# Kernel tuning notes

Measured on AMD Instinct MI355X. Metric: run time of the kernel, lower is better.

## Reference

```python
import jax, jax.numpy as jnp
from jax import lax
import numpy as np

B, T, C = 4, 2048, 1024
H = 4                      # num_heads
D = C // H                 # head_dim
EPS_N = 1e-6               # normalizer eps in scan
EPS_GN = 1e-5              # GroupNorm eps (torch default)


def setup_inputs() -> dict:
    key = jax.random.key(0)
    ks = jax.random.split(key, 8)
    s = 0.02
    return {
        "x": jax.random.normal(ks[0], (B, T, C), jnp.float32),
        "conv_w": jax.random.normal(ks[1], (C, 1, 4), jnp.float32) * s,
        "conv_b": jax.random.normal(ks[2], (C,), jnp.float32) * s,
        "wx_w": jax.random.normal(ks[3], (4 * C, C), jnp.float32) * s,
        "wx_b": jax.random.normal(ks[4], (4 * C,), jnp.float32) * s,
        "gn_w": jnp.ones((C,), jnp.float32),
        "gn_b": jnp.zeros((C,), jnp.float32),
        "out_w": jax.random.normal(ks[5], (C, C), jnp.float32) * s,
        "out_b": jax.random.normal(ks[6], (C,), jnp.float32) * s,
    }


def _slstm_scan(i_g, f_g, z_g, o_g):
    # all inputs (B,T,H,D); scan over time
    def step(carry, g):
        c, n, m = carry
        i_t, f_t, z_t, o_t = g
        m_t = jnp.maximum(f_t + m, i_t)
        i_p = jnp.exp(i_t - m_t)
        f_p = jnp.exp(f_t + m - m_t)
        c_t = f_p * c + i_p * z_t
        n_t = f_p * n + i_p
        h_t = jax.nn.sigmoid(o_t) * (c_t / (n_t + EPS_N))
        return (c_t, n_t, m_t), h_t

    tfirst = lambda a: jnp.transpose(a, (1, 0, 2, 3))  # (T,B,H,D)
    init = (jnp.zeros((B, H, D), i_g.dtype),
            jnp.ones((B, H, D), i_g.dtype),
            jnp.zeros((B, H, D), i_g.dtype))
    _, h_seq = lax.scan(step, init, (tfirst(i_g), tfirst(f_g), tfirst(z_g), tfirst(o_g)))
    return jnp.transpose(h_seq, (1, 0, 2, 3))  # (B,T,H,D)


def reference(x, conv_w, conv_b, wx_w, wx_b, gn_w, gn_b, out_w, out_b):
    # causal depthwise conv (torch pad=3 both sides, sliced to first T == left pad 3)
    xc = jnp.transpose(x, (0, 2, 1))  # (B,C,T)
    xc = lax.conv_general_dilated(
        xc, conv_w, window_strides=(1,), padding=[(3, 0)],
        dimension_numbers=("NCH", "OIH", "NCH"), feature_group_count=C)
    xc = jax.nn.silu(xc + conv_b[None, :, None])
    xc = jnp.transpose(xc, (0, 2, 1))  # (B,T,C)

    gates = jnp.einsum("btc,gc->btg", xc, wx_w) + wx_b  # (B,T,4C)
    gates = gates.reshape(B, T, 4, H, D)
    i_g, f_g, z_g, o_g = (gates[:, :, k] for k in range(4))
    z_g = jnp.tanh(z_g)

    h = _slstm_scan(i_g, f_g, z_g, o_g).reshape(B, T, C)

    # GroupNorm(H groups) over (B,C,T): normalize per (batch, group) over (D, T)
    hg = h.reshape(B, T, H, D)
    mean = hg.mean(axis=(1, 3), keepdims=True)
    var = hg.var(axis=(1, 3), keepdims=True)
    hn = ((hg - mean) / jnp.sqrt(var + EPS_GN)).reshape(B, T, C)
    hn = hn * gn_w + gn_b

    out = jnp.einsum("btc,oc->bto", hn, out_w) + out_b
    return out + x  # dropout is identity at inference
```

## Files before the change

### kernel.cpp

```cpp
#include <hip/hip_runtime.h>

#define B_ 4
#define T_ 2048
#define C_ 1024
#define H_ 4
#define D_ 256
#define M_ (B_*T_)
#define N1_ (4*C_)
#define K_ C_
#define LANES_ (B_*C_)
#define CHUNK_ 32
#define NCHUNK_ (T_/CHUNK_)

typedef unsigned short u16;
typedef unsigned int u32;
typedef __bf16 bf16x8 __attribute__((ext_vector_type(8)));
typedef float f32x4 __attribute__((ext_vector_type(4)));
typedef float vf4 __attribute__((ext_vector_type(4)));
typedef unsigned short u16x4 __attribute__((ext_vector_type(4)));
typedef unsigned short u16x8 __attribute__((ext_vector_type(8)));

__device__ __forceinline__ u16 f2bf(float f) {
  union { float f; u32 u; } v; v.f = f;
  u32 u = v.u;
  u32 r = (u + 0x7FFFu + ((u >> 16) & 1u)) >> 16;
  return (u16)r;
}
__device__ __forceinline__ float b2f(u16 h) {
  union { u32 u; float f; } v; v.u = ((u32)h) << 16;
  return v.f;
}

#define NCAST_ ((N1_*K_ + C_*C_) / 2048)

__global__ void prep_kernel(const float* __restrict__ wx_w, const float* __restrict__ out_w,
                            u16* __restrict__ w1p, u16* __restrict__ w2,
                            const float* __restrict__ x, const float* __restrict__ cw,
                            const float* __restrict__ cb, u16* __restrict__ xc,
                            float* __restrict__ stats) {
  if (blockIdx.x < NCAST_) {
    int i8 = (blockIdx.x * 256 + threadIdx.x) * 8;
    u16x8 o;
    if (i8 < N1_ * K_) {
      int n = i8 >> 10, k8 = i8 & 1023;
      const float* src = wx_w + (size_t)(((n & 3) << 10) | (n >> 2)) * K_ + k8;
      vf4 a = *(const vf4*)src;
      vf4 b = *(const vf4*)(src + 4);
#pragma unroll
      for (int j = 0; j < 4; ++j) { o[j] = f2bf(a[j]); o[j + 4] = f2bf(b[j]); }
      *(u16x8*)(w1p + i8) = o;
    } else {
      int j8 = i8 - N1_ * K_;
      vf4 a = *(const vf4*)(out_w + j8);
      vf4 b = *(const vf4*)(out_w + j8 + 4);
#pragma unroll
      for (int j = 0; j < 4; ++j) { o[j] = f2bf(a[j]); o[j + 4] = f2bf(b[j]); }
      *(u16x8*)(w2 + j8) = o;
    }
    return;
  }
  if (blockIdx.x == NCAST_ && threadIdx.x < 32) stats[threadIdx.x] = 0.f;
  int i4 = ((blockIdx.x - NCAST_) * 256 + threadIdx.x) * 4;
  int c = i4 & (C_ - 1);
  int t = (i4 >> 10) & (T_ - 1);
  vf4 acc = *(const vf4*)(cb + c);
  vf4 w0 = *(const vf4*)(cw + (size_t)c * 4);
  vf4 w1 = *(const vf4*)(cw + (size_t)(c + 1) * 4);
  vf4 w2v = *(const vf4*)(cw + (size_t)(c + 2) * 4);
  vf4 w3 = *(const vf4*)(cw + (size_t)(c + 3) * 4);
#pragma unroll
  for (int k = 0; k < 4; ++k) {
    if (t - 3 + k >= 0) {
      vf4 xv = *(const vf4*)(x + (size_t)i4 + (size_t)(k - 3) * C_);
      acc[0] = fmaf(w0[k], xv[0], acc[0]);
      acc[1] = fmaf(w1[k], xv[1], acc[1]);
      acc[2] = fmaf(w2v[k], xv[2], acc[2]);
      acc[3] = fmaf(w3[k], xv[3], acc[3]);
    }
  }
  u16x4 o;
#pragma unroll
  for (int j = 0; j < 4; ++j) {
    float s = acc[j] / (1.f + __expf(-acc[j]));
    o[j] = f2bf(s);
  }
  *(u16x4*)(xc + i4) = o;
}

template <int EPI>
__global__ __launch_bounds__(256, 3)
void gemm_bt(const u16* __restrict__ A, const u16* __restrict__ Bw,
             const float* __restrict__ bias, const float* __restrict__ resid,
             u16* __restrict__ obf, float* __restrict__ of32,
             f32x4* __restrict__ sSum, int M, int N, int K)
{
  __shared__ __align__(16) u16 smem[128 * 136];
  u16* a_s = smem;
  u16* b_s = smem + 128 * 64;

  const int tid  = threadIdx.x;
  const int lane = tid & 63;
  const int l15  = lane & 15;
  const int q    = lane >> 4;
  const int wave = tid >> 6;
  const int wm   = (wave >> 1) * 64;
  const int wn   = (wave & 1) * 64;
  const int bm   = blockIdx.y * 128;
  const int bn   = blockIdx.x * 128;

  const int srow   = wave * 8 + (lane >> 3);
  const int schunk = lane & 7;

  float bias4[4];
#pragma unroll
  for (int sn = 0; sn < 4; ++sn) {
    int gcol = bn + wn + sn * 16 + l15;
    bias4[sn] = (EPI == 0) ? bias[((gcol & 3) << 10) | (gcol >> 2)] : bias[gcol];
  }
  const bool zlane = (EPI == 0) && ((l15 & 3) == 2);

  f32x4 acc[4][4];
#pragma unroll
  for (int i = 0; i < 4; ++i)
#pragma unroll
    for (int j = 0; j < 4; ++j) acc[i][j] = (f32x4){0.f, 0.f, 0.f, 0.f};

  for (int k0 = 0; k0 < K; k0 += 64) {
#pragma unroll
    for (int i = 0; i < 4; ++i) {
      int r = i * 32 + srow;
      int lc = schunk ^ (r & 7);
      const u16* ga = A  + (size_t)(bm + r) * K + k0 + lc * 8;
      const u16* gb = Bw + (size_t)(bn + r) * K + k0 + lc * 8;
      __builtin_amdgcn_global_load_lds(
          (const __attribute__((address_space(1))) u32*)ga,
          (__attribute__((address_space(3))) u32*)&a_s[(i * 32 + wave * 8) * 64],
          16, 0, 0);
      __builtin_amdgcn_global_load_lds(
          (const __attribute__((address_space(1))) u32*)gb,
          (__attribute__((address_space(3))) u32*)&b_s[(i * 32 + wave * 8) * 64],
          16, 0, 0);
    }
    __syncthreads();
#pragma unroll
    for (int kk = 0; kk < 64; kk += 32) {
      const int kc = kk >> 3;
      bf16x8 af[4], bfr[4];
#pragma unroll
      for (int s = 0; s < 4; ++s) {
        int ra = wm + s * 16 + l15;
        int ph = (kc + q) ^ (ra & 7);
        af[s] = *(const bf16x8*)&a_s[ra * 64 + ph * 8];
      }
#pragma unroll
      for (int s = 0; s < 4; ++s) {
        int rb = wn + s * 16 + l15;
        int ph = (kc + q) ^ (rb & 7);
        bfr[s] = *(const bf16x8*)&b_s[rb * 64 + ph * 8];
      }
#pragma unroll
      for (int sm = 0; sm < 4; ++sm)
#pragma unroll
        for (int sn = 0; sn < 4; ++sn)
          acc[sm][sn] = __builtin_amdgcn_mfma_f32_16x16x32_bf16(af[sm], bfr[sn], acc[sm][sn], 0, 0, 0);
    }
    __syncthreads();
  }

  if (EPI == 0) {
#pragma unroll
    for (int smi = 0; smi < 4; ++smi) {
#pragma unroll
      for (int r = 0; r < 4; ++r) {
        int lrow = wm + smi * 16 + q * 4 + r;
#pragma unroll
        for (int sni = 0; sni < 4; ++sni) {
          int lcol = wn + sni * 16 + l15;
          float v = acc[smi][sni][r] + bias4[sni];
          if (zlane) {
            float e = __expf(2.f * v);
            v = (e - 1.f) / (e + 1.f);
          }
          smem[lrow * 136 + lcol] = f2bf(v);
        }
      }
    }
    __syncthreads();
#pragma unroll
    for (int it = 0; it < 8; ++it) {
      int flat = it * 256 + tid;
      int row = flat >> 4;
      int ch  = flat & 15;
      u16x8 vv = *(const u16x8*)&smem[row * 136 + ch * 8];
      *(u16x8*)(obf + (size_t)(bm + row) * N + bn + ch * 8) = vv;
    }
    if (tid < 128) {
      int ch = tid & 31, ck = tid >> 5;
      const u16* sp = smem + (ck * 32) * 136 + ch * 4;
      float F = 0.f, Mx = -1e30f, aBc = 0.f, aBn = 0.f;
#pragma unroll 8
      for (int t = 0; t < CHUNK_; ++t) {
        u16x4 gv = *(const u16x4*)(sp + t * 136);
        float i_t = b2f(gv[0]), f_t = b2f(gv[1]), z_t = b2f(gv[2]);
        float Mf = Mx + f_t;
        float Mn = fmaxf(Mf, i_t);
        float ea = __expf(Mf - Mn), eb = __expf(i_t - Mn);
        aBc = ea * aBc + eb * z_t;
        aBn = ea * aBn + eb;
        F += f_t; Mx = Mn;
      }
      int b = bm >> 11;
      int s = ((bm & 2047) >> 5) + ck;
      int cg = (bn >> 2) + ch;
      sSum[(size_t)s * LANES_ + b * C_ + cg] = (f32x4){F, Mx, aBc, aBn};
    }
  } else {
    float* fs = (float*)smem;
#pragma unroll
    for (int h = 0; h < 2; ++h) {
      __syncthreads();
#pragma unroll
      for (int smi2 = 0; smi2 < 2; ++smi2) {
        int smi = 2 * h + smi2;
#pragma unroll
        for (int r = 0; r < 4; ++r) {
          int slot = (wm >> 1) + smi2 * 16 + q * 4 + r;
#pragma unroll
          for (int sni = 0; sni < 4; ++sni) {
            int lcol = wn + sni * 16 + l15;
            fs[slot * 132 + lcol] = acc[smi][sni][r] + bias4[sni];
          }
        }
      }
      __syncthreads();
#pragma unroll
      for (int it = 0; it < 8; ++it) {
        int flat = it * 256 + tid;
        int slot = flat >> 5;
        int c4 = (flat & 31) * 4;
        int absrow = bm + ((slot & 32) << 1) + (h << 5) + (slot & 31);
        vf4 v = *(const vf4*)&fs[slot * 132 + c4];
        vf4 rv = *(const vf4*)(resid + (size_t)absrow * N + bn + c4);
        v[0] += rv[0]; v[1] += rv[1]; v[2] += rv[2]; v[3] += rv[3];
        *(vf4*)(of32 + (size_t)absrow * N + bn + c4) = v;
      }
    }
  }
}

__global__ void scan_prefix(const f32x4* __restrict__ sSum, f32x4* __restrict__ iSt) {
  int l = blockIdx.x * 256 + threadIdx.x;
  float ct = 0.f, nt = 1.f, mt = 0.f;
#pragma unroll 8
  for (int s = 0; s < NCHUNK_; ++s) {
    int idx = s * LANES_ + l;
    f32x4 S = sSum[idx];
    iSt[idx] = (f32x4){ct, nt, mt, 0.f};
    float mf = mt + S[0];
    float mn = fmaxf(mf, S[1]);
    float a = __expf(mf - mn);
    float bcoef = __expf(S[1] - mn);
    ct = a * ct + bcoef * S[2];
    nt = a * nt + bcoef * S[3];
    mt = mn;
  }
}

__global__ void scan_passB(const u16* __restrict__ gates, const f32x4* __restrict__ iSt,
                           u16* __restrict__ h, float* __restrict__ stats) {
  int tid = blockIdx.x * 256 + threadIdx.x;
  int lp = tid & 2047;
  int s = tid >> 11;
  int b = lp >> 9;
  int c2 = (lp & 511) * 2;
  const u16* g = gates + ((size_t)(b * T_ + s * CHUNK_) * C_ + c2) * 4;
  u16* hp = h + (size_t)(b * T_ + s * CHUNK_) * C_ + c2;
  int idx = s * LANES_ + b * C_ + c2;
  f32x4 S0 = iSt[idx], S1 = iSt[idx + 1];
  float cc0 = S0[0], nn0 = S0[1], mm0 = S0[2];
  float cc1 = S1[0], nn1 = S1[1], mm1 = S1[2];
  float ls = 0.f, lq = 0.f;
#pragma unroll 4
  for (int t = 0; t < CHUNK_; ++t) {
    u16x8 gv = *(const u16x8*)(g + (size_t)t * C_ * 4);
    float h0, h1;
    {
      float i_t = b2f(gv[0]), f_t = b2f(gv[1]), z_t = b2f(gv[2]), o_t = b2f(gv[3]);
      float m_new = fmaxf(f_t + mm0, i_t);
      float i_p = __expf(i_t - m_new);
      float f_p = __expf(f_t + mm0 - m_new);
      cc0 = f_p * cc0 + i_p * z_t;
      nn0 = f_p * nn0 + i_p;
      mm0 = m_new;
      float sig_o = 1.f / (1.f + __expf(-o_t));
      h0 = sig_o * (cc0 / (nn0 + 1e-6f));
    }
    {
      float i_t = b2f(gv[4]), f_t = b2f(gv[5]), z_t = b2f(gv[6]), o_t = b2f(gv[7]);
      float m_new = fmaxf(f_t + mm1, i_t);
      float i_p = __expf(i_t - m_new);
      float f_p = __expf(f_t + mm1 - m_new);
      cc1 = f_p * cc1 + i_p * z_t;
      nn1 = f_p * nn1 + i_p;
      mm1 = m_new;
      float sig_o = 1.f / (1.f + __expf(-o_t));
      h1 = sig_o * (cc1 / (nn1 + 1e-6f));
    }
    u16 hb0 = f2bf(h0), hb1 = f2bf(h1);
    float v0 = b2f(hb0), v1 = b2f(hb1);
    ls += v0 + v1; lq += v0 * v0 + v1 * v1;
    *(u32*)(hp + (size_t)t * C_) = (u32)hb0 | ((u32)hb1 << 16);
  }
  __shared__ float rs[256], rq[256];
  int thr = threadIdx.x;
  rs[thr] = ls; rq[thr] = lq;
  __syncthreads();
  for (int off = 64; off > 0; off >>= 1) {
    if ((thr & 127) < off) { rs[thr] += rs[thr + off]; rq[thr] += rq[thr + off]; }
    __syncthreads();
  }
  if ((thr & 127) == 0) {
    int grp = b * 4 + (c2 >> 8);
    atomicAdd(&stats[grp * 2 + 0], rs[thr]);
    atomicAdd(&stats[grp * 2 + 1], rq[thr]);
  }
}

__global__ void norm_kernel(const u16* __restrict__ h, const float* __restrict__ stats,
                            const float* __restrict__ gn_w, const float* __restrict__ gn_b,
                            u16* __restrict__ hn) {
  int i8 = (blockIdx.x * 256 + threadIdx.x) * 8;
  int c = i8 & (C_ - 1);
  int b = i8 >> 21;
  int grp = b * 4 + (c >> 8);
  const float inv_n = 1.f / (float)(T_ * D_);
  float mean = stats[grp * 2 + 0] * inv_n;
  float var  = stats[grp * 2 + 1] * inv_n - mean * mean;
  float rstd = rsqrtf(var + 1e-5f);
  u16x8 hv = *(const u16x8*)(h + i8);
  vf4 w0 = *(const vf4*)(gn_w + c), w1 = *(const vf4*)(gn_w + c + 4);
  vf4 b0 = *(const vf4*)(gn_b + c), b1 = *(const vf4*)(gn_b + c + 4);
  u16x8 o;
#pragma unroll
  for (int j = 0; j < 4; ++j) {
    o[j]     = f2bf((b2f(hv[j])     - mean) * rstd * w0[j] + b0[j]);
    o[j + 4] = f2bf((b2f(hv[j + 4]) - mean) * rstd * w1[j] + b1[j]);
  }
  *(u16x8*)(hn + i8) = o;
}

extern "C" void kernel_launch(void* const* d_in, const int* in_sizes, int n_in,
                              void* d_out, int out_size, void* d_ws, size_t ws_size,
                              hipStream_t stream) {
  const float* x      = (const float*)d_in[0];
  const float* conv_w = (const float*)d_in[1];
  const float* conv_b = (const float*)d_in[2];
  const float* wx_w   = (const float*)d_in[3];
  const float* wx_b   = (const float*)d_in[4];
  const float* gn_w   = (const float*)d_in[5];
  const float* gn_b   = (const float*)d_in[6];
  const float* out_w  = (const float*)d_in[7];
  const float* out_b  = (const float*)d_in[8];
  float* out = (float*)d_out;

  char* p = (char*)d_ws;
  u16* xc    = (u16*)p; p += (size_t)M_ * K_ * 2;
  u16* w1    = (u16*)p; p += (size_t)N1_ * K_ * 2;
  u16* w2    = (u16*)p; p += (size_t)C_ * C_ * 2;
  u16* gts   = (u16*)p; p += (size_t)M_ * N1_ * 2;
  u16* hb    = (u16*)p; p += (size_t)M_ * C_ * 2;
  u16* hn    = (u16*)p; p += (size_t)M_ * C_ * 2;
  float* stats = (float*)p; p += 256;
  const int nsum = LANES_ * NCHUNK_;
  f32x4* sSum = (f32x4*)p; p += (size_t)nsum * 16;
  f32x4* iSt  = (f32x4*)p; p += (size_t)nsum * 16;

  prep_kernel<<<NCAST_ + (M_ * C_) / 1024, 256, 0, stream>>>(
      wx_w, out_w, w1, w2, x, conv_w, conv_b, xc, stats);

  gemm_bt<0><<<dim3(N1_ / 128, M_ / 128), 256, 0, stream>>>(
      xc, w1, wx_b, nullptr, gts, nullptr, sSum, M_, N1_, K_);

  scan_prefix<<<LANES_ / 256, 256, 0, stream>>>(sSum, iSt);
  scan_passB<<<(2048 * NCHUNK_) / 256, 256, 0, stream>>>(gts, iSt, hb, stats);

  norm_kernel<<<(M_ * C_) / 2048, 256, 0, stream>>>(hb, stats, gn_w, gn_b, hn);

  gemm_bt<1><<<dim3(C_ / 128, M_ / 128), 256, 0, stream>>>(
      hn, w2, out_b, x, nullptr, out, nullptr, M_, C_, K_);
}
```

Before: 268.2 us.

## Replace gates GEMM with 256x256-tile, 512-thread, 4-stage LDS-pipelined kernel

Adds a dedicated gates GEMM that uses 256x256 output tiles with 8 waves and a 4-buffer ring of direct global-to-LDS loads, staged three slices ahead. Counted vmcnt waits, barrier sandwiches and setprio around the MFMA bursts are meant to overlap loads with compute. The bias, tanh and chunk-summary epilogue is kept. Larger tiles increase data reuse and cut global traffic per FLOP. This uses about 132KB of LDS and many accumulator registers, which limits occupancy, and it hardcodes shapes and a block-swizzle mapping.

After: 281.6 us. 5.0% more time.

```diff
diff --git a/kernel.cpp b/kernel.cpp
--- a/kernel.cpp
+++ b/kernel.cpp
@@ -85,6 +85,182 @@
     o[j] = f2bf(s);
   }
   *(u16x4*)(xc + i4) = o;
+}
+
+
+__device__ __forceinline__ void stage32(const u16* __restrict__ G, int rowBase, int ks,
+                                        u16* dstPart, int wave, int lane) {
+#pragma unroll
+  for (int r = 0; r < 2; ++r) {
+    int R = r * 64 + wave * 8 + (lane >> 3);
+    int c = (lane & 7) ^ (R & 7);
+    int grow = 2 * R + (c >> 2);
+    int koff = ks * 32 + (c & 3) * 8;
+    const u16* src = G + (size_t)(rowBase + grow) * K_ + koff;
+    __builtin_amdgcn_global_load_lds(
+        (const __attribute__((address_space(1))) u32*)src,
+        (__attribute__((address_space(3))) u32*)&dstPart[(r * 64 + wave * 8) * 64],
+        16, 0, 0);
+  }
+}
+
+#define BARRIER_SANDWICH() do {                   \
+    __builtin_amdgcn_sched_barrier(0);            \
+    __builtin_amdgcn_s_barrier();                 \
+    __builtin_amdgcn_sched_barrier(0);            \
+  } while (0)
+
+#define VM8 asm volatile("s_waitcnt vmcnt(8)" ::: "memory")
+#define VM4 asm volatile("s_waitcnt vmcnt(4)" ::: "memory")
+#define VM0 asm volatile("s_waitcnt vmcnt(0)" ::: "memory")
+#define VMNONE ((void)0)
+
+#define GEMM_SLICE(sIdx, DO_STAGE, VMW) do {                                     \
+    u16* base_ = smem + ((sIdx) & 3) * 16384;                                    \
+    const u16* aP_ = base_;                                                      \
+    const u16* bP_ = base_ + 8192;                                               \
+    bf16x8 af_[4], bf_[4];                                                       \
+    _Pragma("unroll")                                                            \
+    for (int sub = 0; sub < 4; ++sub) {                                          \
+      int ra = wr * 128 + sub * 16 + l15;                                        \
+      int Ra = ra >> 1;                                                          \
+      int ca = (((ra & 1) << 2) | q) ^ (Ra & 7);                                 \
+      af_[sub] = *(const bf16x8*)&aP_[Ra * 64 + ca * 8];                         \
+      int rb = wc * 64 + sub * 16 + l15;                                         \
+      int Rb = rb >> 1;                                                          \
+      int cb = (((rb & 1) << 2) | q) ^ (Rb & 7);                                 \
+      bf_[sub] = *(const bf16x8*)&bP_[Rb * 64 + cb * 8];                         \
+    }                                                                            \
+    if (DO_STAGE) stage32(A, bm, (sIdx) + 3,                                     \
+        smem + (((sIdx) + 3) & 3) * 16384, wave, lane);                          \
+    BARRIER_SANDWICH();                                                          \
+    __builtin_amdgcn_s_setprio(1);                                               \
+    _Pragma("unroll")                                                            \
+    for (int sm = 0; sm < 4; ++sm)                                               \
+      _Pragma("unroll")                                                          \
+      for (int sn = 0; sn < 4; ++sn)                                             \
+        acc[sm][sn] = __builtin_amdgcn_mfma_f32_16x16x32_bf16(af_[sm], bf_[sn],  \
+                                                              acc[sm][sn], 0, 0, 0); \
+    __builtin_amdgcn_s_setprio(0);                                               \
+    BARRIER_SANDWICH();                                                          \
+    _Pragma("unroll")                                                            \
+    for (int sub = 0; sub < 4; ++sub) {                                          \
+      int ra = wr * 128 + 64 + sub * 16 + l15;                                   \
+      int Ra = ra >> 1;                                                          \
+      int ca = (((ra & 1) << 2) | q) ^ (Ra & 7);                                 \
+      af_[sub] = *(const bf16x8*)&aP_[Ra * 64 + ca * 8];                         \
+    }                                                                            \
+    if (DO_STAGE) stage32(Bw, bn, (sIdx) + 3,                                    \
+        smem + (((sIdx) + 3) & 3) * 16384 + 8192, wave, lane);                   \
+    BARRIER_SANDWICH();                                                          \
+    __builtin_amdgcn_s_setprio(1);                                               \
+    _Pragma("unroll")                                                            \
+    for (int sm = 0; sm < 4; ++sm)                                               \
+      _Pragma("unroll")                                                          \
+      for (int sn = 0; sn < 4; ++sn)                                             \
+        acc[4 + sm][sn] = __builtin_amdgcn_mfma_f32_16x16x32_bf16(af_[sm], bf_[sn], \
+                                                          acc[4 + sm][sn], 0, 0, 0); \
+    __builtin_amdgcn_s_setprio(0);                                               \
+    VMW;                                                                         \
+    BARRIER_SANDWICH();                                                          \
+  } while (0)
+
+__global__ __launch_bounds__(512, 2)
+void gemm256_gates(const u16* __restrict__ A, const u16* __restrict__ Bw,
+                   const float* __restrict__ bias,
+                   u16* __restrict__ obf, f32x4* __restrict__ sSum)
+{
+  __shared__ __align__(16) u16 smem[67584];
+
+  const int tid  = threadIdx.x;
+  const int lane = tid & 63;
+  const int l15  = lane & 15;
+  const int q    = lane >> 4;
+  const int wave = tid >> 6;
+  const int wr   = wave >> 2;
+  const int wc   = wave & 3;
+
+  const int bid = blockIdx.y * 16 + blockIdx.x;
+  const int swz = (bid & 7) * 64 + (bid >> 3);
+  const int bm = (swz >> 4) * 256;
+  const int bn = (swz & 15) * 256;
+
+  float bias4[4];
+#pragma unroll
+  for (int sn = 0; sn < 4; ++sn) {
+    int gcol = bn + wc * 64 + sn * 16 + l15;
+    bias4[sn] = bias[((gcol & 3) << 10) | (gcol >> 2)];
+  }
+  const bool zlane = ((l15 & 3) == 2);
+
+  f32x4 acc[8][4];
+#pragma unroll
+  for (int i = 0; i < 8; ++i)
+#pragma unroll
+    for (int j = 0; j < 4; ++j) acc[i][j] = (f32x4){0.f, 0.f, 0.f, 0.f};
+
+#pragma unroll
+  for (int s3 = 0; s3 < 3; ++s3) {
+    stage32(A,  bm, s3, smem + s3 * 16384,        wave, lane);
+    stage32(Bw, bn, s3, smem + s3 * 16384 + 8192, wave, lane);
+  }
+  asm volatile("s_waitcnt vmcnt(8)" ::: "memory");
+  BARRIER_SANDWICH();
+
+#pragma unroll 1
+  for (int s = 0; s < 29; ++s) GEMM_SLICE(s, true, VM8);
+  GEMM_SLICE(29, false, VM4);
+  GEMM_SLICE(30, false, VM0);
+  GEMM_SLICE(31, false, VMNONE);
+
+#pragma unroll
+  for (int sm = 0; sm < 8; ++sm) {
+#pragma unroll
+    for (int r = 0; r < 4; ++r) {
+      int lrow = wr * 128 + sm * 16 + q * 4 + r;
+#pragma unroll
+      for (int sn = 0; sn < 4; ++sn) {
+        int lcol = wc * 64 + sn * 16 + l15;
+        float v = acc[sm][sn][r] + bias4[sn];
+        if (zlane) {
+          float e = __expf(2.f * v);
+          v = (e - 1.f) / (e + 1.f);
+        }
+        smem[lrow * 264 + lcol] = f2bf(v);
+      }
+    }
+  }
+  __syncthreads();
+
+#pragma unroll
+  for (int it = 0; it < 16; ++it) {
+    int flat = it * 512 + tid;
+    int row = flat >> 5;
+    int ch8 = flat & 31;
+    u16x8 vv = *(const u16x8*)&smem[row * 264 + ch8 * 8];
+    *(u16x8*)(obf + (size_t)(bm + row) * N1_ + bn + ch8 * 8) = vv;
+  }
+
+  {
+    int ch = tid & 63, ck = tid >> 6;
+    const u16* sp = smem + (ck * 32) * 264 + ch * 4;
+    float F = 0.f, Mx = -1e30f, aBc = 0.f, aBn = 0.f;
+#pragma unroll 8
+    for (int t = 0; t < CHUNK_; ++t) {
+      u16x4 gv = *(const u16x4*)(sp + t * 264);
+      float i_t = b2f(gv[0]), f_t = b2f(gv[1]), z_t = b2f(gv[2]);
+      float Mf = Mx + f_t;
+      float Mn = fmaxf(Mf, i_t);
+      float ea = __expf(Mf - Mn), eb = __expf(i_t - Mn);
+      aBc = ea * aBc + eb * z_t;
+      aBn = ea * aBn + eb;
+      F += f_t; Mx = Mn;
+    }
+    int b = bm >> 11;
+    int s_ = ((bm & 2047) >> 5) + ck;
+    int cg = (bn >> 2) + ch;
+    sSum[(size_t)s_ * LANES_ + b * C_ + cg] = (f32x4){F, Mx, aBc, aBn};
+  }
 }
 
 template <int EPI>
@@ -378,8 +554,8 @@
   prep_kernel<<<NCAST_ + (M_ * C_) / 1024, 256, 0, stream>>>(
       wx_w, out_w, w1, w2, x, conv_w, conv_b, xc, stats);
 
-  gemm_bt<0><<<dim3(N1_ / 128, M_ / 128), 256, 0, stream>>>(
-      xc, w1, wx_b, nullptr, gts, nullptr, sSum, M_, N1_, K_);
+  gemm256_gates<<<dim3(N1_ / 256, M_ / 256), 512, 0, stream>>>(
+      xc, w1, wx_b, gts, sSum);
 
   scan_prefix<<<LANES_ / 256, 256, 0, stream>>>(sSum, iSt);
   scan_passB<<<(2048 * NCHUNK_) / 256, 256, 0, stream>>>(gts, iSt, hb, stats);
```

## Fold GroupNorm affine into per-batch output projection weights and bias

Applied to the files above, without the earlier changes.

Replaces the elementwise GroupNorm kernel, which read h and wrote a normalized copy, with a small kernel that folds mean, rstd, gamma and beta into per-batch scaled bf16 copies of out_w plus an adjusted bias. The output GEMM then reads the raw h buffer directly and selects the batch's weights and bias by row block. This removes a full read/write pass over the activation, and the out_w bf16 cast moves out of prep. In exchange it writes and reads four weight copies (8 MB) and applies the scale in bf16 weights rather than activations, which slightly changes rounding.

New measurement: 279.0 us (median of 2 runs). 1.04x slower.

```diff
diff --git a/kernel.cpp b/kernel.cpp
--- a/kernel.cpp
+++ b/kernel.cpp
@@ -31,32 +31,23 @@
   return v.f;
 }
 
-#define NCAST_ ((N1_*K_ + C_*C_) / 2048)
-
-__global__ void prep_kernel(const float* __restrict__ wx_w, const float* __restrict__ out_w,
-                            u16* __restrict__ w1p, u16* __restrict__ w2,
+#define NCAST_ ((N1_*K_) / 2048)
+
+__global__ void prep_kernel(const float* __restrict__ wx_w,
+                            u16* __restrict__ w1p,
                             const float* __restrict__ x, const float* __restrict__ cw,
                             const float* __restrict__ cb, u16* __restrict__ xc,
                             float* __restrict__ stats) {
   if (blockIdx.x < NCAST_) {
     int i8 = (blockIdx.x * 256 + threadIdx.x) * 8;
+    int n = i8 >> 10, k8 = i8 & 1023;
+    const float* src = wx_w + (size_t)(((n & 3) << 10) | (n >> 2)) * K_ + k8;
+    vf4 a = *(const vf4*)src;
+    vf4 b = *(const vf4*)(src + 4);
     u16x8 o;
-    if (i8 < N1_ * K_) {
-      int n = i8 >> 10, k8 = i8 & 1023;
-      const float* src = wx_w + (size_t)(((n & 3) << 10) | (n >> 2)) * K_ + k8;
-      vf4 a = *(const vf4*)src;
-      vf4 b = *(const vf4*)(src + 4);
-#pragma unroll
-      for (int j = 0; j < 4; ++j) { o[j] = f2bf(a[j]); o[j + 4] = f2bf(b[j]); }
-      *(u16x8*)(w1p + i8) = o;
-    } else {
-      int j8 = i8 - N1_ * K_;
-      vf4 a = *(const vf4*)(out_w + j8);
-      vf4 b = *(const vf4*)(out_w + j8 + 4);
-#pragma unroll
-      for (int j = 0; j < 4; ++j) { o[j] = f2bf(a[j]); o[j + 4] = f2bf(b[j]); }
-      *(u16x8*)(w2 + j8) = o;
-    }
+#pragma unroll
+    for (int j = 0; j < 4; ++j) { o[j] = f2bf(a[j]); o[j + 4] = f2bf(b[j]); }
+    *(u16x8*)(w1p + i8) = o;
     return;
   }
   if (blockIdx.x == NCAST_ && threadIdx.x < 32) stats[threadIdx.x] = 0.f;
@@ -107,6 +98,12 @@
   const int wn   = (wave & 1) * 64;
   const int bm   = blockIdx.y * 128;
   const int bn   = blockIdx.x * 128;
+
+  if (EPI == 1) {
+    int batch = bm >> 11;
+    Bw   += (size_t)batch * N * K;
+    bias += (size_t)batch << 10;
+  }
 
   const int srow   = wave * 8 + (lane >> 3);
   const int schunk = lane & 7;
@@ -326,27 +323,44 @@
   }
 }
 
-__global__ void norm_kernel(const u16* __restrict__ h, const float* __restrict__ stats,
-                            const float* __restrict__ gn_w, const float* __restrict__ gn_b,
-                            u16* __restrict__ hn) {
-  int i8 = (blockIdx.x * 256 + threadIdx.x) * 8;
-  int c = i8 & (C_ - 1);
-  int b = i8 >> 21;
-  int grp = b * 4 + (c >> 8);
+__global__ void gn_fold(const float* __restrict__ out_w, const float* __restrict__ stats,
+                        const float* __restrict__ gn_w, const float* __restrict__ gn_b,
+                        const float* __restrict__ out_b,
+                        u16* __restrict__ w2p, float* __restrict__ biasp) {
+  const int batch = blockIdx.y;
+  const int o = blockIdx.x * 16 + (threadIdx.x >> 4);
+  const int seg = threadIdx.x & 15;
+  const int c0 = seg * 64;
+  const int grp = batch * 4 + (c0 >> 8);
   const float inv_n = 1.f / (float)(T_ * D_);
   float mean = stats[grp * 2 + 0] * inv_n;
   float var  = stats[grp * 2 + 1] * inv_n - mean * mean;
   float rstd = rsqrtf(var + 1e-5f);
-  u16x8 hv = *(const u16x8*)(h + i8);
-  vf4 w0 = *(const vf4*)(gn_w + c), w1 = *(const vf4*)(gn_w + c + 4);
-  vf4 b0 = *(const vf4*)(gn_b + c), b1 = *(const vf4*)(gn_b + c + 4);
-  u16x8 o;
-#pragma unroll
-  for (int j = 0; j < 4; ++j) {
-    o[j]     = f2bf((b2f(hv[j])     - mean) * rstd * w0[j] + b0[j]);
-    o[j + 4] = f2bf((b2f(hv[j + 4]) - mean) * rstd * w1[j] + b1[j]);
-  }
-  *(u16x8*)(hn + i8) = o;
+  const float* wrow = out_w + (size_t)o * C_;
+  u16* wdst = w2p + ((size_t)batch * C_ + o) * C_;
+  float acc = 0.f;
+#pragma unroll 4
+  for (int c = c0; c < c0 + 64; c += 4) {
+    vf4 w  = *(const vf4*)(wrow + c);
+    vf4 gw = *(const vf4*)(gn_w + c);
+    vf4 gb = *(const vf4*)(gn_b + c);
+    u16x4 ov;
+#pragma unroll
+    for (int j = 0; j < 4; ++j) {
+      float s1 = rstd * gw[j];
+      ov[j] = f2bf(s1 * w[j]);
+      acc = fmaf(gb[j] - mean * s1, w[j], acc);
+    }
+    *(u16x4*)(wdst + c) = ov;
+  }
+  __shared__ float red[256];
+  red[threadIdx.x] = acc;
+  __syncthreads();
+  for (int off = 8; off > 0; off >>= 1) {
+    if (seg < off) red[threadIdx.x] += red[threadIdx.x + off];
+    __syncthreads();
+  }
+  if (seg == 0) biasp[batch * C_ + o] = out_b[o] + red[threadIdx.x];
 }
 
 extern "C" void kernel_launch(void* const* d_in, const int* in_sizes, int n_in,
@@ -366,17 +380,17 @@
   char* p = (char*)d_ws;
   u16* xc    = (u16*)p; p += (size_t)M_ * K_ * 2;
   u16* w1    = (u16*)p; p += (size_t)N1_ * K_ * 2;
-  u16* w2    = (u16*)p; p += (size_t)C_ * C_ * 2;
   u16* gts   = (u16*)p; p += (size_t)M_ * N1_ * 2;
   u16* hb    = (u16*)p; p += (size_t)M_ * C_ * 2;
-  u16* hn    = (u16*)p; p += (size_t)M_ * C_ * 2;
+  u16* w2p   = (u16*)p; p += (size_t)B_ * C_ * C_ * 2;
+  float* biasp = (float*)p; p += (size_t)B_ * C_ * 4;
   float* stats = (float*)p; p += 256;
   const int nsum = LANES_ * NCHUNK_;
   f32x4* sSum = (f32x4*)p; p += (size_t)nsum * 16;
   f32x4* iSt  = (f32x4*)p; p += (size_t)nsum * 16;
 
   prep_kernel<<<NCAST_ + (M_ * C_) / 1024, 256, 0, stream>>>(
-      wx_w, out_w, w1, w2, x, conv_w, conv_b, xc, stats);
+      wx_w, w1, x, conv_w, conv_b, xc, stats);
 
   gemm_bt<0><<<dim3(N1_ / 128, M_ / 128), 256, 0, stream>>>(
       xc, w1, wx_b, nullptr, gts, nullptr, sSum, M_, N1_, K_);
@@ -384,8 +398,9 @@
   scan_prefix<<<LANES_ / 256, 256, 0, stream>>>(sSum, iSt);
   scan_passB<<<(2048 * NCHUNK_) / 256, 256, 0, stream>>>(gts, iSt, hb, stats);
 
-  norm_kernel<<<(M_ * C_) / 2048, 256, 0, stream>>>(hb, stats, gn_w, gn_b, hn);
+  gn_fold<<<dim3(C_ / 16, B_), 256, 0, stream>>>(
+      out_w, stats, gn_w, gn_b, out_b, w2p, biasp);
 
   gemm_bt<1><<<dim3(C_ / 128, M_ / 128), 256, 0, stream>>>(
-      hn, w2, out_b, x, nullptr, out, nullptr, M_, C_, K_);
-}
+      hb, w2p, biasp, x, nullptr, out, nullptr, M_, C_, K_);
+}
```
